# Performance work log

Hardware: AMD Instinct MI355X
Metric: run time of the kernel (lower is better)

The kernel has to match this reference:

```python
import jax, jax.numpy as jnp
import numpy as np

B, S, H = 4, 2048, 2048
N_HEADS, KV_HEADS, RANK = 16, 8, 64
HEAD_DIM = H // N_HEADS          # 128
N_REP = N_HEADS // KV_HEADS      # 2
NEG = -1e9


def setup_inputs() -> dict:
    key = jax.random.key(0)
    ks = jax.random.split(key, 6)
    hidden_states = jax.random.normal(ks[0], (B, S, H), dtype=jnp.float32)
    # additive causal mask, broadcast over heads: [B,1,S,S]
    causal = jnp.tril(jnp.ones((S, S), dtype=bool))
    attention_mask = jnp.where(causal, 0.0, NEG).astype(jnp.float32)
    attention_mask = jnp.broadcast_to(attention_mask[None, None], (B, 1, S, S))
    sc = 1.0 / np.sqrt(H)
    Wq = jax.random.normal(ks[1], (H, RANK), dtype=jnp.float32) * sc
    Wk = jax.random.normal(ks[2], (H, RANK), dtype=jnp.float32) * sc
    Wv = jax.random.normal(ks[3], (H, KV_HEADS * HEAD_DIM), dtype=jnp.float32) * sc
    Wo = jax.random.normal(ks[4], (H, H), dtype=jnp.float32) * sc
    return {"hidden_states": hidden_states, "attention_mask": attention_mask,
            "Wq": Wq, "Wk": Wk, "Wv": Wv, "Wo": Wo}


def reference(hidden_states, attention_mask, Wq, Wk, Wv, Wo):
    b, s, h = hidden_states.shape
    # low-rank CP factors shared across heads: [B,S,R]
    q = hidden_states @ Wq
    k = hidden_states @ Wk
    # values with GQA: [B, kv_heads, S, head_dim] -> repeat to [B, n_heads, S, head_dim]
    v = (hidden_states @ Wv).reshape(b, s, KV_HEADS, HEAD_DIM).transpose(0, 2, 1, 3)
    v = jnp.repeat(v, N_REP, axis=1)
    # CP circuit over the (i,j) grid: scores[b,i,j] = sum_r q[b,i,r] * k[b,j,r]
    # (Hadamard over embedding factors gathered at grid indices, SumLayer with unit
    #  weights over rank; the all-ones head factor multiplies by 1). Head-shared.
    scores = jnp.einsum('bir,bjr->bij', q, k)[:, None]  # [B,1,S,S]
    scores = scores + attention_mask                     # additive causal mask
    probs = jax.nn.softmax(scores.astype(jnp.float32), axis=-1).astype(v.dtype)
    # attn_probs @ V, broadcasting the head-shared probs over heads
    ctx = jnp.einsum('bij,bhjd->bhid', probs[:, 0], v)   # [B,H,S,D]
    ctx = ctx.transpose(0, 2, 1, 3).reshape(b, s, h)
    return ctx @ Wo
```

## Files before the change

kernel.cpp:

```cpp
#include <hip/hip_runtime.h>

#define B_ 4
#define S_ 2048
#define H_ 2048
#define R_ 64
#define DKV_ 1024

typedef __attribute__((ext_vector_type(8))) short s16x8;
typedef __attribute__((ext_vector_type(4))) float f32x4v;

__device__ __forceinline__ unsigned short f2bf(float x) {
  unsigned int u = __builtin_bit_cast(unsigned int, x);
  u += 0x7FFF + ((u >> 16) & 1);
  return (unsigned short)(u >> 16);
}
__device__ __forceinline__ float bf2f(unsigned short h) {
  unsigned int u = ((unsigned int)h) << 16;
  return __builtin_bit_cast(float, u);
}

__device__ __forceinline__ void gl_lds16(const void* g, void* l) {
  __builtin_amdgcn_global_load_lds(
      (const __attribute__((address_space(1))) unsigned int*)g,
      (__attribute__((address_space(3))) unsigned int*)l, 16, 0, 0);
}

__device__ __forceinline__ int swz_off(int m, int kb) {
  int L = m >> 1;
  int slot = ((m & 1) << 2) | (kb >> 4);
  int sp = slot ^ (L & 7);
  return (L << 7) | (sp << 4) | (kb & 15);
}

__global__ __launch_bounds__(256) void k_transpose_bf16(const float* __restrict__ in,
    unsigned short* __restrict__ out, int rows, int cols) {
  __shared__ float tile[32][33];
  int c0 = blockIdx.x * 32, r0 = blockIdx.y * 32;
  int tx = threadIdx.x & 31, ty = threadIdx.x >> 5;
  for (int i = 0; i < 4; ++i)
    tile[ty + i * 8][tx] = in[(size_t)(r0 + ty + i * 8) * cols + c0 + tx];
  __syncthreads();
  for (int i = 0; i < 4; ++i)
    out[(size_t)(c0 + ty + i * 8) * rows + r0 + tx] = f2bf(tile[tx][ty + i * 8]);
}

__global__ __launch_bounds__(256) void k_build_wqkt(const float* __restrict__ Wq,
    const float* __restrict__ Wk, unsigned short* __restrict__ hiT,
    unsigned short* __restrict__ loT) {
  __shared__ float tile[32][33];
  int k0 = blockIdx.x * 32, n0 = blockIdx.y * 32;
  const float* W = (n0 < 64) ? Wq : Wk;
  int nb = n0 & 63;
  int tx = threadIdx.x & 31, ty = threadIdx.x >> 5;
  for (int i = 0; i < 4; ++i)
    tile[ty + i * 8][tx] = W[(size_t)(k0 + ty + i * 8) * R_ + nb + tx];
  __syncthreads();
  for (int i = 0; i < 4; ++i) {
    float v = tile[tx][ty + i * 8];
    unsigned short h = f2bf(v);
    size_t idx = (size_t)(n0 + ty + i * 8) * H_ + k0 + tx;
    hiT[idx] = h;
    loT[idx] = f2bf(v - bf2f(h));
  }
}

__global__ __launch_bounds__(256) void k_build_wot(const float* __restrict__ Wo,
                                                   unsigned short* __restrict__ WoT) {
  __shared__ float tile[32][33];
  int n0 = blockIdx.x * 32, r0 = blockIdx.y * 32;
  int h1b = 256 * (r0 >> 7) + (r0 & 127);
  int tx = threadIdx.x & 31, ty = threadIdx.x >> 5;
  for (int i = 0; i < 4; ++i) {
    int dr = ty + i * 8;
    tile[dr][tx] = Wo[(size_t)(h1b + dr) * H_ + n0 + tx] +
                   Wo[(size_t)(h1b + 128 + dr) * H_ + n0 + tx];
  }
  __syncthreads();
  for (int i = 0; i < 4; ++i)
    WoT[(size_t)(n0 + ty + i * 8) * DKV_ + r0 + tx] = f2bf(tile[tx][ty + i * 8]);
}

__global__ __launch_bounds__(256) void k_qk_fused(
    const float* __restrict__ hs,
    const unsigned short* __restrict__ Bhi, const unsigned short* __restrict__ Blo,
    unsigned short* __restrict__ hsb,
    unsigned short* __restrict__ qkh, unsigned short* __restrict__ qkl) {
  constexpr int TQK = 20480;
  __shared__ __attribute__((aligned(16))) char lds[3 * TQK];
  int m0 = blockIdx.x * 32;
  int t = threadIdx.x;
  int lane = t & 63, wave = t >> 6;
  int lr = lane & 15, kb = (lane >> 4) << 4;

  int arow = t >> 3;
  int acol = (t & 7) << 2;
  const float* asrc = hs + (size_t)(m0 + arow) * H_ + acol;
  unsigned short* hdst = hsb + (size_t)(m0 + arow) * H_ + acol;
  int adst = swz_off(arow, ((t & 7) >> 1) << 4) + ((t & 1) << 3);

  auto stageB = [&](int kt, char* base) {
    int k0 = kt << 5;
#pragma unroll
    for (int c = 0; c < 2; ++c) {
      int q = c * 256 + t;
      int L = q >> 3;
      int slot = (q & 7) ^ (L & 7);
      int n = (L << 1) | (slot >> 2);
      int ke = (slot & 3) << 3;
      gl_lds16(Bhi + (size_t)n * H_ + k0 + ke, base + 4096 + q * 16);
    }
#pragma unroll
    for (int c = 0; c < 2; ++c) {
      int q = c * 256 + t;
      int L = q >> 3;
      int slot = (q & 7) ^ (L & 7);
      int n = (L << 1) | (slot >> 2);
      int ke = (slot & 3) << 3;
      gl_lds16(Blo + (size_t)n * H_ + k0 + ke, base + 12288 + q * 16);
    }
  };

  auto convA = [&](const float4& v, char* wbuf, int kt) {
    ushort4 h, l;
    h.x = f2bf(v.x); h.y = f2bf(v.y); h.z = f2bf(v.z); h.w = f2bf(v.w);
    l.x = f2bf(v.x - bf2f(h.x)); l.y = f2bf(v.y - bf2f(h.y));
    l.z = f2bf(v.z - bf2f(h.z)); l.w = f2bf(v.w - bf2f(h.w));
    *(ushort4*)(wbuf + adst) = h;
    *(ushort4*)(wbuf + 2048 + adst) = l;
    *(ushort4*)(hdst + (size_t)kt * 32) = h;
  };

  float4 Rcur, Rnext;
  Rcur = *(const float4*)(asrc);
  stageB(0, &lds[0]);
  Rnext = *(const float4*)(asrc + 32);
  stageB(1, &lds[TQK]);
  convA(Rcur, &lds[0], 0);
  Rcur = Rnext;

  f32x4v acc[2][2] = {};
  int cur = 0, wb = 1, sb = 2;
  for (int kt = 0; kt < 64; ++kt) {
    __builtin_amdgcn_sched_barrier(0);
    if (kt < 62) asm volatile("s_waitcnt vmcnt(6) lgkmcnt(0)" ::: "memory");
    else asm volatile("s_waitcnt vmcnt(0) lgkmcnt(0)" ::: "memory");
    __builtin_amdgcn_s_barrier();
    __builtin_amdgcn_sched_barrier(0);
    if (kt + 2 < 64) {
      Rnext = *(const float4*)(asrc + (size_t)(kt + 2) * 32);
      stageB(kt + 2, &lds[sb * TQK]);
    }
    const char* base = &lds[cur * TQK];
    s16x8 ah[2], al[2], bh[2], bl[2];
#pragma unroll
    for (int m = 0; m < 2; ++m) {
      int o = swz_off(m * 16 + lr, kb);
      ah[m] = *(const s16x8*)(base + o);
      al[m] = *(const s16x8*)(base + 2048 + o);
    }
#pragma unroll
    for (int n = 0; n < 2; ++n) {
      int o = swz_off(wave * 32 + n * 16 + lr, kb);
      bh[n] = *(const s16x8*)(base + 4096 + o);
      bl[n] = *(const s16x8*)(base + 12288 + o);
    }
    if (kt + 1 < 64) convA(Rcur, &lds[wb * TQK], kt + 1);
    __builtin_amdgcn_s_setprio(1);
#pragma unroll
    for (int m = 0; m < 2; ++m)
#pragma unroll
      for (int n = 0; n < 2; ++n) {
        acc[m][n] = __builtin_amdgcn_mfma_f32_16x16x32_bf16(ah[m], bh[n], acc[m][n], 0, 0, 0);
        acc[m][n] = __builtin_amdgcn_mfma_f32_16x16x32_bf16(ah[m], bl[n], acc[m][n], 0, 0, 0);
        acc[m][n] = __builtin_amdgcn_mfma_f32_16x16x32_bf16(al[m], bh[n], acc[m][n], 0, 0, 0);
      }
    __builtin_amdgcn_s_setprio(0);
    Rcur = Rnext;
    cur = (cur == 2) ? 0 : cur + 1;
    wb = (wb == 2) ? 0 : wb + 1;
    sb = (sb == 2) ? 0 : sb + 1;
  }
  for (int m = 0; m < 2; ++m) {
    int lrow = m * 16 + ((lane >> 4) << 2);
    for (int n = 0; n < 2; ++n) {
      int lcol = wave * 32 + n * 16 + lr;
      for (int r = 0; r < 4; ++r) {
        float v = acc[m][n][r];
        unsigned short h = f2bf(v);
        size_t idx = (size_t)(m0 + lrow + r) * 128 + lcol;
        qkh[idx] = h;
        qkl[idx] = f2bf(v - bf2f(h));
      }
    }
  }
}

__global__ __launch_bounds__(512, 4) void k_attn_fused(
    const unsigned short* __restrict__ qkh, const unsigned short* __restrict__ qkl,
    const unsigned short* __restrict__ VT, unsigned short* __restrict__ ctx) {
  constexpr int TILEB = 24576;
  __shared__ __attribute__((aligned(16))) char lds[3 * TILEB + 4096 + 256];
  char* Pt = &lds[3 * TILEB];
  float* rs = (float*)&lds[3 * TILEB + 4096];

  int t = threadIdx.x;
  int gx = gridDim.x;
  int x = blockIdx.x;
  int bx = (x & 1) ? (gx - 1 - (x >> 1)) : (x >> 1);
  if (blockIdx.z & 2) bx = gx - 1 - bx;
  int z = blockIdx.z;
  int m0 = bx * 64, d0 = blockIdx.y * 256;

  int lane = t & 63, wave = t >> 6;
  int sm = wave >> 1, sn = wave & 1;
  int wr = wave >> 2, wc = wave & 3;
  int kb = (lane >> 4) << 4;

  const unsigned short* qh = qkh + (size_t)z * S_ * 128;
  const unsigned short* ql = qkl + (size_t)z * S_ * 128;

  s16x8 qfh[2], qfl[2];
  {
    size_t rq = (size_t)(m0 + sm * 16 + (lane & 15)) * 128 + ((lane >> 4) << 3);
    qfh[0] = *(const s16x8*)(qh + rq);
    qfh[1] = *(const s16x8*)(qh + rq + 32);
    qfl[0] = *(const s16x8*)(ql + rq);
    qfl[1] = *(const s16x8*)(ql + rq + 32);
  }

  auto stage = [&](int kt, int buf) {
    int j0 = kt << 5;
    char* base = &lds[buf * TILEB];
    {
      int q = t & 127;
      int L = q >> 3;
      int slot = (q & 7) ^ (L & 7);
      int jr = (L << 1) | (slot >> 2);
      int ke = (slot & 3) << 3;
      int sub = t >> 7;
      const unsigned short* src = ((sub < 2) ? qh : ql) +
          (size_t)(j0 + jr) * 128 + 64 + ((sub & 1) << 5) + ke;
      gl_lds16(src, base + sub * 2048 + q * 16);
    }
    char* vb = base + 8192;
#pragma unroll
    for (int c = 0; c < 2; ++c) {
      int q = c * 512 + t;
      int L = q >> 3;
      int slot = (q & 7) ^ (L & 7);
      int dr = (L << 1) | (slot >> 2);
      int ke = (slot & 3) << 3;
      gl_lds16(VT + (size_t)(d0 + dr) * (B_ * S_) + (size_t)z * S_ + j0 + ke,
               vb + q * 16);
    }
  };

  if (t < 64) rs[t] = 0.f;
  int NT = (m0 + 64) >> 5;
  stage(0, 0);
  stage(1, 1);

  int jrow = sn * 16 + (lane & 15);
  int koffs = swz_off(jrow, kb);
  int paoff[2], voff[4];
#pragma unroll
  for (int mf = 0; mf < 2; ++mf)
    paoff[mf] = swz_off(wr * 32 + mf * 16 + (lane & 15), kb);
#pragma unroll
  for (int nf = 0; nf < 4; ++nf)
    voff[nf] = swz_off(wc * 64 + nf * 16 + (lane & 15), kb);

  float ps[4] = {0.f, 0.f, 0.f, 0.f};
  f32x4v accp[2][4] = {};
  int prow = sm * 16 + ((lane >> 4) << 2);
  int pcol = sn * 16 + (lane & 15);

  int cur = 0, nxt = 2;
  for (int kt = 0; kt < NT; ++kt) {
    __builtin_amdgcn_sched_barrier(0);
    if (kt + 1 < NT) asm volatile("s_waitcnt vmcnt(3) lgkmcnt(0)" ::: "memory");
    else asm volatile("s_waitcnt vmcnt(0) lgkmcnt(0)" ::: "memory");
    __builtin_amdgcn_s_barrier();
    __builtin_amdgcn_sched_barrier(0);
    if (kt + 2 < NT) stage(kt + 2, nxt);
    const char* base = &lds[cur * TILEB];
    s16x8 kh[2], kl[2];
    kh[0] = *(const s16x8*)(base + koffs);
    kh[1] = *(const s16x8*)(base + 2048 + koffs);
    kl[0] = *(const s16x8*)(base + 4096 + koffs);
    kl[1] = *(const s16x8*)(base + 6144 + koffs);
    f32x4v s = {};
#pragma unroll
    for (int ks = 0; ks < 2; ++ks) {
      s = __builtin_amdgcn_mfma_f32_16x16x32_bf16(qfh[ks], kh[ks], s, 0, 0, 0);
      s = __builtin_amdgcn_mfma_f32_16x16x32_bf16(qfh[ks], kl[ks], s, 0, 0, 0);
      s = __builtin_amdgcn_mfma_f32_16x16x32_bf16(qfl[ks], kh[ks], s, 0, 0, 0);
    }
    int jg = (kt << 5) + pcol;
    int ig = m0 + prow;
#pragma unroll
    for (int r = 0; r < 4; ++r) {
      float p = (jg <= ig + r) ? __expf(s[r]) : 0.f;
      ps[r] += p;
      *(unsigned short*)(Pt + swz_off(prow + r, pcol * 2)) = f2bf(p);
    }
    __builtin_amdgcn_sched_barrier(0);
    asm volatile("s_waitcnt lgkmcnt(0)" ::: "memory");
    __builtin_amdgcn_s_barrier();
    __builtin_amdgcn_sched_barrier(0);
    s16x8 pa[2], vf[4];
#pragma unroll
    for (int mf = 0; mf < 2; ++mf) pa[mf] = *(const s16x8*)(Pt + paoff[mf]);
    const char* vbase = base + 8192;
#pragma unroll
    for (int nf = 0; nf < 4; ++nf) vf[nf] = *(const s16x8*)(vbase + voff[nf]);
    __builtin_amdgcn_s_setprio(1);
#pragma unroll
    for (int mf = 0; mf < 2; ++mf)
#pragma unroll
      for (int nf = 0; nf < 4; ++nf)
        accp[mf][nf] =
            __builtin_amdgcn_mfma_f32_16x16x32_bf16(pa[mf], vf[nf], accp[mf][nf], 0, 0, 0);
    __builtin_amdgcn_s_setprio(0);
    cur = (cur == 2) ? 0 : cur + 1;
    nxt = (nxt == 2) ? 0 : nxt + 1;
  }

#pragma unroll
  for (int r = 0; r < 4; ++r) {
    float v = ps[r];
    for (int msk = 1; msk < 16; msk <<= 1) v += __shfl_xor(v, msk, 64);
    if ((lane & 15) == 0) atomicAdd(&rs[prow + r], v);
  }
  __syncthreads();

  unsigned short* Cp = ctx + (size_t)(z * S_ + m0) * DKV_ + d0;
#pragma unroll
  for (int mf = 0; mf < 2; ++mf) {
    int lr0 = wr * 32 + mf * 16 + ((lane >> 4) << 2);
#pragma unroll
    for (int nf = 0; nf < 4; ++nf) {
      int lc = wc * 64 + nf * 16 + (lane & 15);
#pragma unroll
      for (int r = 0; r < 4; ++r) {
        float sc = 1.f / rs[lr0 + r];
        Cp[(size_t)(lr0 + r) * DKV_ + lc] = f2bf(accp[mf][nf][r] * sc);
      }
    }
  }
}

template <int BM, int BN, bool TRANS_OUT, bool OUT_BF16>
__global__ __launch_bounds__(512, 4) void k_gemm256(
    const unsigned short* __restrict__ A, int lda,
    const unsigned short* __restrict__ BT, int ldbt,
    void* __restrict__ C, int ldc, int K) {
  constexpr int ABYTES = BM * 64;
  constexpr int BBYTES = BN * 64;
  constexpr int TILEB = ABYTES + BBYTES;
  constexpr int WARPS_M = 4;
  constexpr int WARPS_N = 2;
  constexpr int WM = BM / WARPS_M;
  constexpr int WN = BN / WARPS_N;
  constexpr int MF = WM / 16;
  constexpr int NF = WN / 16;
  constexpr int LPS = BM / 128 + BN / 128;
  __shared__ __attribute__((aligned(16))) char lds[3 * TILEB];

  int t = threadIdx.x;
  int gx = gridDim.x;
  int id = blockIdx.y * gx + blockIdx.x;
  int cpx = gx >> 3;
  int xcd = id & 7, rr = id >> 3;
  int bx = xcd * cpx + rr % cpx;
  int by = rr / cpx;
  int m0 = bx * BM, n0 = by * BN;

  const unsigned short* Ab = A + (size_t)m0 * lda;
  const unsigned short* Bb = BT + (size_t)n0 * ldbt;

  int lane = t & 63, wave = t >> 6;
  int wr = wave / WARPS_N, wc = wave % WARPS_N;
  int kb = (lane >> 4) << 4;
  int aoff[MF], boff[NF];
#pragma unroll
  for (int mf = 0; mf < MF; ++mf)
    aoff[mf] = swz_off(wr * WM + mf * 16 + (lane & 15), kb);
#pragma unroll
  for (int nf = 0; nf < NF; ++nf)
    boff[nf] = swz_off(wc * WN + nf * 16 + (lane & 15), kb);

  int NT = K >> 5;

  auto stage = [&](int kt, int buf) {
    int k0 = kt << 5;
    char* la = &lds[buf * TILEB];
    char* lb = la + ABYTES;
#pragma unroll
    for (int c = 0; c < BM / 128; ++c) {
      int q = c * 512 + t;
      int L = q >> 3;
      int slot = (q & 7) ^ (L & 7);
      int m = (L << 1) | (slot >> 2);
      int ke = (slot & 3) << 3;
      gl_lds16(Ab + (size_t)m * lda + k0 + ke, la + q * 16);
    }
#pragma unroll
    for (int c = 0; c < BN / 128; ++c) {
      int q = c * 512 + t;
      int L = q >> 3;
      int slot = (q & 7) ^ (L & 7);
      int n = (L << 1) | (slot >> 2);
      int ke = (slot & 3) << 3;
      gl_lds16(Bb + (size_t)n * ldbt + k0 + ke, lb + q * 16);
    }
  };

  f32x4v acc[MF][NF] = {};
  stage(0, 0);
  if (NT > 1) stage(1, 1);
  int cur = 0, nxt = 2;
  for (int kt = 0; kt < NT; ++kt) {
    __builtin_amdgcn_sched_barrier(0);
    if (kt + 1 < NT) {
      if constexpr (LPS == 2) asm volatile("s_waitcnt vmcnt(2)" ::: "memory");
      else asm volatile("s_waitcnt vmcnt(3)" ::: "memory");
    } else {
      asm volatile("s_waitcnt vmcnt(0)" ::: "memory");
    }
    __builtin_amdgcn_s_barrier();
    __builtin_amdgcn_sched_barrier(0);
    if (kt + 2 < NT) stage(kt + 2, nxt);
    const char* la = &lds[cur * TILEB];
    const char* lb = la + ABYTES;
    s16x8 af[MF], bf[NF];
#pragma unroll
    for (int mf = 0; mf < MF; ++mf) af[mf] = *(const s16x8*)(la + aoff[mf]);
#pragma unroll
    for (int nf = 0; nf < NF; ++nf) bf[nf] = *(const s16x8*)(lb + boff[nf]);
    __builtin_amdgcn_s_setprio(1);
#pragma unroll
    for (int mf = 0; mf < MF; ++mf)
#pragma unroll
      for (int nf = 0; nf < NF; ++nf)
        acc[mf][nf] =
            __builtin_amdgcn_mfma_f32_16x16x32_bf16(af[mf], bf[nf], acc[mf][nf], 0, 0, 0);
    __builtin_amdgcn_s_setprio(0);
    cur = (cur == 2) ? 0 : cur + 1;
    nxt = (nxt == 2) ? 0 : nxt + 1;
  }

#pragma unroll
  for (int mf = 0; mf < MF; ++mf) {
    int lrow = wr * WM + mf * 16 + ((lane >> 4) << 2);
#pragma unroll
    for (int nf = 0; nf < NF; ++nf) {
      int lcol = wc * WN + nf * 16 + (lane & 15);
      f32x4v v = acc[mf][nf];
      if (TRANS_OUT) {
        ushort4 o;
        o.x = f2bf(v[0]); o.y = f2bf(v[1]); o.z = f2bf(v[2]); o.w = f2bf(v[3]);
        unsigned short* Cp = (unsigned short*)C;
        *(ushort4*)&Cp[(size_t)(n0 + lcol) * ldc + m0 + lrow] = o;
      } else {
#pragma unroll
        for (int r = 0; r < 4; ++r) {
          if (OUT_BF16) {
            unsigned short* Cp = (unsigned short*)C;
            Cp[(size_t)(m0 + lrow + r) * ldc + n0 + lcol] = f2bf(v[r]);
          } else {
            float* Cp = (float*)C;
            Cp[(size_t)(m0 + lrow + r) * ldc + n0 + lcol] = v[r];
          }
        }
      }
    }
  }
}

extern "C" void kernel_launch(void* const* d_in, const int* in_sizes, int n_in,
                              void* d_out, int out_size, void* d_ws, size_t ws_size,
                              hipStream_t stream) {
  const float* hs = (const float*)d_in[0];
  const float* Wq = (const float*)d_in[2];
  const float* Wk = (const float*)d_in[3];
  const float* Wv = (const float*)d_in[4];
  const float* Wo = (const float*)d_in[5];
  float* out = (float*)d_out;

  char* w = (char*)d_ws;
  unsigned short* hsb = (unsigned short*)w; w += (size_t)B_ * S_ * H_ * 2;
  unsigned short* WvT = (unsigned short*)w; w += (size_t)DKV_ * H_ * 2;
  unsigned short* WoT = (unsigned short*)w; w += (size_t)H_ * DKV_ * 2;
  unsigned short* WqkTh = (unsigned short*)w; w += (size_t)128 * H_ * 2;
  unsigned short* WqkTl = (unsigned short*)w; w += (size_t)128 * H_ * 2;
  unsigned short* VT  = (unsigned short*)w; w += (size_t)DKV_ * B_ * S_ * 2;
  unsigned short* ctx = (unsigned short*)w; w += (size_t)B_ * S_ * DKV_ * 2;
  unsigned short* qkh = (unsigned short*)w; w += (size_t)B_ * S_ * 128 * 2;
  unsigned short* qkl = (unsigned short*)w; w += (size_t)B_ * S_ * 128 * 2;

  k_transpose_bf16<<<dim3(DKV_ / 32, H_ / 32), 256, 0, stream>>>(Wv, WvT, H_, DKV_);
  k_build_wot<<<dim3(H_ / 32, DKV_ / 32), 256, 0, stream>>>(Wo, WoT);
  k_build_wqkt<<<dim3(H_ / 32, 4), 256, 0, stream>>>(Wq, Wk, WqkTh, WqkTl);
  k_qk_fused<<<B_ * S_ / 32, 256, 0, stream>>>(hs, WqkTh, WqkTl, hsb, qkh, qkl);
  k_gemm256<256, 128, true, true>
      <<<dim3(B_ * S_ / 256, DKV_ / 128), 512, 0, stream>>>(
      hsb, H_, WvT, H_, VT, B_ * S_, H_);
  k_attn_fused<<<dim3(32, 4, B_), 512, 0, stream>>>(qkh, qkl, VT, ctx);
  k_gemm256<256, 128, false, false>
      <<<dim3(B_ * S_ / 256, H_ / 128), 512, 0, stream>>>(
      ctx, DKV_, WoT, DKV_, out, H_, DKV_);
}
```

Baseline: 199.5 us.

## Split QK projection over K into four chunks with a separate reduction kernel

The fused hidden-state-to-QK projection kernel is split along the K dimension into four 512-wide chunks with 512-thread blocks, each wave owning a 16-column slice, and double buffering replaces triple buffering. This gives four times as many blocks to fill the GPU, since the original grid of 256 blocks likely underused the CUs. Partial fp32 sums go to a new workspace buffer and a second kernel adds them and produces the hi/lo bf16 outputs. The cost is an extra launch plus writing and re-reading 16 MB of partials.

```diff
diff --git a/kernel.cpp b/kernel.cpp
--- a/kernel.cpp
+++ b/kernel.cpp
@@ -80,119 +80,116 @@
     WoT[(size_t)(n0 + ty + i * 8) * DKV_ + r0 + tx] = f2bf(tile[tx][ty + i * 8]);
 }
 
-__global__ __launch_bounds__(256) void k_qk_fused(
+__global__ __launch_bounds__(512, 8) void k_qk_split(
     const float* __restrict__ hs,
     const unsigned short* __restrict__ Bhi, const unsigned short* __restrict__ Blo,
-    unsigned short* __restrict__ hsb,
-    unsigned short* __restrict__ qkh, unsigned short* __restrict__ qkl) {
+    unsigned short* __restrict__ hsb, float* __restrict__ part) {
   constexpr int TQK = 20480;
-  __shared__ __attribute__((aligned(16))) char lds[3 * TQK];
+  __shared__ __attribute__((aligned(16))) char lds[2 * TQK];
   int m0 = blockIdx.x * 32;
+  int kc0 = blockIdx.y * 512;
   int t = threadIdx.x;
   int lane = t & 63, wave = t >> 6;
   int lr = lane & 15, kb = (lane >> 4) << 4;
 
-  int arow = t >> 3;
-  int acol = (t & 7) << 2;
-  const float* asrc = hs + (size_t)(m0 + arow) * H_ + acol;
-  unsigned short* hdst = hsb + (size_t)(m0 + arow) * H_ + acol;
-  int adst = swz_off(arow, ((t & 7) >> 1) << 4) + ((t & 1) << 3);
+  int arow = t >> 4;
+  const float* asrc = hs + (size_t)(m0 + arow) * H_ + kc0 + ((t & 15) << 1);
+  unsigned short* hdst = hsb + (size_t)(m0 + arow) * H_ + kc0 + ((t & 15) << 1);
+  int adst = swz_off(arow, (t & 15) << 2);
 
   auto stageB = [&](int kt, char* base) {
-    int k0 = kt << 5;
-#pragma unroll
-    for (int c = 0; c < 2; ++c) {
-      int q = c * 256 + t;
-      int L = q >> 3;
-      int slot = (q & 7) ^ (L & 7);
-      int n = (L << 1) | (slot >> 2);
-      int ke = (slot & 3) << 3;
-      gl_lds16(Bhi + (size_t)n * H_ + k0 + ke, base + 4096 + q * 16);
-    }
-#pragma unroll
-    for (int c = 0; c < 2; ++c) {
-      int q = c * 256 + t;
-      int L = q >> 3;
-      int slot = (q & 7) ^ (L & 7);
-      int n = (L << 1) | (slot >> 2);
-      int ke = (slot & 3) << 3;
-      gl_lds16(Blo + (size_t)n * H_ + k0 + ke, base + 12288 + q * 16);
-    }
+    int k0 = kc0 + (kt << 5);
+    int L = t >> 3;
+    int slot = (t & 7) ^ (L & 7);
+    int n = (L << 1) | (slot >> 2);
+    int ke = (slot & 3) << 3;
+    gl_lds16(Bhi + (size_t)n * H_ + k0 + ke, base + 4096 + t * 16);
+    gl_lds16(Blo + (size_t)n * H_ + k0 + ke, base + 12288 + t * 16);
   };
 
-  auto convA = [&](const float4& v, char* wbuf, int kt) {
-    ushort4 h, l;
-    h.x = f2bf(v.x); h.y = f2bf(v.y); h.z = f2bf(v.z); h.w = f2bf(v.w);
+  auto convA = [&](const float2& v, char* wbuf, int kt) {
+    ushort2 h, l;
+    h.x = f2bf(v.x); h.y = f2bf(v.y);
     l.x = f2bf(v.x - bf2f(h.x)); l.y = f2bf(v.y - bf2f(h.y));
-    l.z = f2bf(v.z - bf2f(h.z)); l.w = f2bf(v.w - bf2f(h.w));
-    *(ushort4*)(wbuf + adst) = h;
-    *(ushort4*)(wbuf + 2048 + adst) = l;
-    *(ushort4*)(hdst + (size_t)kt * 32) = h;
+    *(ushort2*)(wbuf + adst) = h;
+    *(ushort2*)(wbuf + 2048 + adst) = l;
+    *(ushort2*)(hdst + (size_t)kt * 32) = h;
   };
 
-  float4 Rcur, Rnext;
-  Rcur = *(const float4*)(asrc);
+  float2 R0 = *(const float2*)(asrc);
   stageB(0, &lds[0]);
-  Rnext = *(const float4*)(asrc + 32);
-  stageB(1, &lds[TQK]);
-  convA(Rcur, &lds[0], 0);
-  Rcur = Rnext;
-
-  f32x4v acc[2][2] = {};
-  int cur = 0, wb = 1, sb = 2;
-  for (int kt = 0; kt < 64; ++kt) {
-    __builtin_amdgcn_sched_barrier(0);
-    if (kt < 62) asm volatile("s_waitcnt vmcnt(6) lgkmcnt(0)" ::: "memory");
+  float2 Rcur = *(const float2*)(asrc + 32);
+  asm volatile("s_waitcnt vmcnt(3)" ::: "memory");
+  convA(R0, &lds[0], 0);
+
+  f32x4v acc[2] = {};
+  for (int kt = 0; kt < 16; ++kt) {
+    char* curb = &lds[(kt & 1) * TQK];
+    char* nxtb = &lds[((kt + 1) & 1) * TQK];
+    if (kt + 1 < 16) stageB(kt + 1, nxtb);
+    float2 Rnext;
+    if (kt + 2 < 16) Rnext = *(const float2*)(asrc + (size_t)(kt + 2) * 32);
+    __builtin_amdgcn_sched_barrier(0);
+    if (kt + 2 < 16) asm volatile("s_waitcnt vmcnt(4) lgkmcnt(0)" ::: "memory");
+    else if (kt + 1 < 16) asm volatile("s_waitcnt vmcnt(3) lgkmcnt(0)" ::: "memory");
     else asm volatile("s_waitcnt vmcnt(0) lgkmcnt(0)" ::: "memory");
     __builtin_amdgcn_s_barrier();
     __builtin_amdgcn_sched_barrier(0);
-    if (kt + 2 < 64) {
-      Rnext = *(const float4*)(asrc + (size_t)(kt + 2) * 32);
-      stageB(kt + 2, &lds[sb * TQK]);
-    }
-    const char* base = &lds[cur * TQK];
-    s16x8 ah[2], al[2], bh[2], bl[2];
+    if (kt + 1 < 16) convA(Rcur, nxtb, kt + 1);
+    Rcur = Rnext;
+    s16x8 ah[2], al[2], bh, bl;
 #pragma unroll
     for (int m = 0; m < 2; ++m) {
       int o = swz_off(m * 16 + lr, kb);
-      ah[m] = *(const s16x8*)(base + o);
-      al[m] = *(const s16x8*)(base + 2048 + o);
-    }
-#pragma unroll
-    for (int n = 0; n < 2; ++n) {
-      int o = swz_off(wave * 32 + n * 16 + lr, kb);
-      bh[n] = *(const s16x8*)(base + 4096 + o);
-      bl[n] = *(const s16x8*)(base + 12288 + o);
-    }
-    if (kt + 1 < 64) convA(Rcur, &lds[wb * TQK], kt + 1);
+      ah[m] = *(const s16x8*)(curb + o);
+      al[m] = *(const s16x8*)(curb + 2048 + o);
+    }
+    {
+      int o = swz_off(wave * 16 + lr, kb);
+      bh = *(const s16x8*)(curb + 4096 + o);
+      bl = *(const s16x8*)(curb + 12288 + o);
+    }
     __builtin_amdgcn_s_setprio(1);
 #pragma unroll
-    for (int m = 0; m < 2; ++m)
-#pragma unroll
-      for (int n = 0; n < 2; ++n) {
-        acc[m][n] = __builtin_amdgcn_mfma_f32_16x16x32_bf16(ah[m], bh[n], acc[m][n], 0, 0, 0);
-        acc[m][n] = __builtin_amdgcn_mfma_f32_16x16x32_bf16(ah[m], bl[n], acc[m][n], 0, 0, 0);
-        acc[m][n] = __builtin_amdgcn_mfma_f32_16x16x32_bf16(al[m], bh[n], acc[m][n], 0, 0, 0);
-      }
+    for (int m = 0; m < 2; ++m) {
+      acc[m] = __builtin_amdgcn_mfma_f32_16x16x32_bf16(ah[m], bh, acc[m], 0, 0, 0);
+      acc[m] = __builtin_amdgcn_mfma_f32_16x16x32_bf16(ah[m], bl, acc[m], 0, 0, 0);
+      acc[m] = __builtin_amdgcn_mfma_f32_16x16x32_bf16(al[m], bh, acc[m], 0, 0, 0);
+    }
     __builtin_amdgcn_s_setprio(0);
-    Rcur = Rnext;
-    cur = (cur == 2) ? 0 : cur + 1;
-    wb = (wb == 2) ? 0 : wb + 1;
-    sb = (sb == 2) ? 0 : sb + 1;
-  }
+  }
+
+  float* Pp = part + (size_t)blockIdx.y * (8192 * 128);
+#pragma unroll
   for (int m = 0; m < 2; ++m) {
     int lrow = m * 16 + ((lane >> 4) << 2);
-    for (int n = 0; n < 2; ++n) {
-      int lcol = wave * 32 + n * 16 + lr;
-      for (int r = 0; r < 4; ++r) {
-        float v = acc[m][n][r];
-        unsigned short h = f2bf(v);
-        size_t idx = (size_t)(m0 + lrow + r) * 128 + lcol;
-        qkh[idx] = h;
-        qkl[idx] = f2bf(v - bf2f(h));
-      }
-    }
-  }
+    int lcol = wave * 16 + lr;
+#pragma unroll
+    for (int r = 0; r < 4; ++r)
+      Pp[(size_t)(m0 + lrow + r) * 128 + lcol] = acc[m][r];
+  }
+}
+
+__global__ __launch_bounds__(256) void k_qk_reduce(const float* __restrict__ part,
+    unsigned short* __restrict__ qkh, unsigned short* __restrict__ qkl) {
+  constexpr size_t CH = (size_t)8192 * 128;
+  size_t i = ((size_t)blockIdx.x * 256 + threadIdx.x) * 4;
+  float4 a = *(const float4*)(part + i);
+  float4 b = *(const float4*)(part + CH + i);
+  float4 c = *(const float4*)(part + 2 * CH + i);
+  float4 d = *(const float4*)(part + 3 * CH + i);
+  float v[4] = {a.x + b.x + c.x + d.x, a.y + b.y + c.y + d.y,
+                a.z + b.z + c.z + d.z, a.w + b.w + c.w + d.w};
+  ushort4 h, l;
+  unsigned short* hp = (unsigned short*)&h;
+  unsigned short* lp = (unsigned short*)&l;
+#pragma unroll
+  for (int r = 0; r < 4; ++r) {
+    hp[r] = f2bf(v[r]);
+    lp[r] = f2bf(v[r] - bf2f(hp[r]));
+  }
+  *(ushort4*)(qkh + i) = h;
+  *(ushort4*)(qkl + i) = l;
 }
 
 __global__ __launch_bounds__(512, 4) void k_attn_fused(
@@ -498,11 +495,13 @@
   unsigned short* ctx = (unsigned short*)w; w += (size_t)B_ * S_ * DKV_ * 2;
   unsigned short* qkh = (unsigned short*)w; w += (size_t)B_ * S_ * 128 * 2;
   unsigned short* qkl = (unsigned short*)w; w += (size_t)B_ * S_ * 128 * 2;
+  float* part = (float*)w; w += (size_t)4 * B_ * S_ * 128 * 4;
 
   k_transpose_bf16<<<dim3(DKV_ / 32, H_ / 32), 256, 0, stream>>>(Wv, WvT, H_, DKV_);
   k_build_wot<<<dim3(H_ / 32, DKV_ / 32), 256, 0, stream>>>(Wo, WoT);
   k_build_wqkt<<<dim3(H_ / 32, 4), 256, 0, stream>>>(Wq, Wk, WqkTh, WqkTl);
-  k_qk_fused<<<B_ * S_ / 32, 256, 0, stream>>>(hs, WqkTh, WqkTl, hsb, qkh, qkl);
+  k_qk_split<<<dim3(B_ * S_ / 32, 4), 512, 0, stream>>>(hs, WqkTh, WqkTl, hsb, part);
+  k_qk_reduce<<<(B_ * S_ * 128) / (256 * 4), 256, 0, stream>>>(part, qkh, qkl);
   k_gemm256<256, 128, true, true>
       <<<dim3(B_ * S_ / 256, DKV_ / 128), 512, 0, stream>>>(
       hsb, H_, WvT, H_, VT, B_ * S_, H_);
```

New measurement: 189.1 us. 5.2% less time.
